# Performance work log

Hardware: AMD Instinct MI355X
Metric: run time of the kernel (lower is better)

Reference implementation:

```python
import jax, jax.numpy as jnp
import numpy as np


def setup_inputs() -> dict:
    key = jax.random.key(0)
    k1, k2, k3 = jax.random.split(key, 3)
    B, F0, D = 8192, 39, 16
    L = 128
    hash_x = jax.random.normal(k1, (B, F0, D), dtype=jnp.float32)
    W0 = jax.random.normal(k2, (F0 * F0, L), dtype=jnp.float32) * 0.05
    W1 = jax.random.normal(k3, (F0 * (L // 2), L), dtype=jnp.float32) * 0.05
    return {"hash_x": hash_x, "W0": W0, "W1": W1}


def reference(hash_x, W0, W1):
    # CIN (Compressed Interaction Network) with layer sizes [128, 128], no bias.
    x0 = hash_x                      # [B, F0, D]
    B, F0, D = x0.shape
    L = W0.shape[1]                  # 128

    # --- layer 0 ---
    # outer product over fields per embedding dim: [B, D, F0, F0] -> flatten (i,j) row-major
    z0 = jnp.einsum('bid,bjd->bdij', x0, x0).reshape(B, D, F0 * F0)
    # conv1d with kernel width 1 == matmul over flattened field-pair dim
    cur0 = jax.nn.relu(jnp.einsum('bdk,kl->bld', z0, W0))   # [B, L, D]
    next_h, direct0 = jnp.split(cur0, 2, axis=1)            # each [B, L/2, D]

    # --- layer 1 (final) ---
    Fk = next_h.shape[1]                                     # L/2 = 64
    z1 = jnp.einsum('bid,bjd->bdij', x0, next_h).reshape(B, D, F0 * Fk)
    cur1 = jax.nn.relu(jnp.einsum('bdk,kl->bld', z1, W1))   # [B, L, D]

    result = jnp.concatenate([direct0, cur1], axis=1)        # [B, L/2 + L, D]
    return jnp.sum(result, axis=-1)                          # [B, 192]
```

## Files before the change

### kernel.cpp

```cpp
#include <hip/hip_runtime.h>
#include <hip/hip_bf16.h>


using short8 = __attribute__((ext_vector_type(8))) short;
using f32x16 = __attribute__((ext_vector_type(16))) float;

#define VS 56
#define V_BYTES (256 * VS * 2)
#define HS 72
#define H_BYTES (256 * HS * 2)
#define BB_OFF (V_BYTES + H_BYTES)
#define SMEM_BYTES (BB_OFF + 8192)

#define NSL0 120
#define NSL1 156
#define NSL  (NSL0 + NSL1)
#define NFRAG (NSL * 256)

__device__ __forceinline__ unsigned short f2bf(float x) {
  __hip_bfloat16 h = __float2bfloat16(x);
  return __builtin_bit_cast(unsigned short, h);
}
__device__ __forceinline__ unsigned cvt2(float lo, float hi) {
  unsigned r;
  asm("v_cvt_pk_bf16_f32 %0, %1, %2" : "=v"(r) : "v"(lo), "v"(hi));
  return r;
}
__device__ __forceinline__ float bf_lo(unsigned w) {
  return __builtin_bit_cast(float, w << 16);
}
__device__ __forceinline__ float bf_hi(unsigned w) {
  return __builtin_bit_cast(float, w & 0xffff0000u);
}
__device__ __forceinline__ float bf2f(unsigned short b) {
  return __builtin_bit_cast(float, ((unsigned)b) << 16);
}
__device__ __forceinline__ short8 mk_a(float vi, uint4 p) {
  uint4 pk;
  pk.x = cvt2(vi * bf_lo(p.x), vi * bf_hi(p.x));
  pk.y = cvt2(vi * bf_lo(p.y), vi * bf_hi(p.y));
  pk.z = cvt2(vi * bf_lo(p.z), vi * bf_hi(p.z));
  pk.w = cvt2(vi * bf_lo(p.w), vi * bf_hi(p.w));
  return __builtin_bit_cast(short8, pk);
}
__device__ __forceinline__ void stage16(const void* g, char* l) {
  __builtin_amdgcn_global_load_lds((const __attribute__((address_space(1))) void*)g,
                                   (__attribute__((address_space(3))) void*)l, 16, 0, 0);
}

__global__ void pack_w(const float* __restrict__ W0, const float* __restrict__ W1,
                       short8* __restrict__ wpk) {
  int fid = blockIdx.x * 256 + threadIdx.x;
  if (fid >= NFRAG) return;
  int lane = fid & 63;
  int t2 = fid >> 6;
  int nb = t2 & 3, s = t2 >> 2;
  int n = nb * 32 + (lane & 31);
  int kb = (lane >> 5) * 8;
  short8 frag;
  #pragma unroll
  for (int ii = 0; ii < 8; ii++) {
    float val;
    if (s < NSL0) {
      int k = s * 16 + kb + ii;
      int i = k / 48, j = k - i * 48;
      val = (i < 39 && j < 39) ? W0[(i * 39 + j) * 128 + n] : 0.f;
    } else {
      int k = (s - NSL0) * 16 + kb + ii;
      int i = k >> 6, j = k & 63;
      val = W1[(i * 64 + j) * 128 + n];
    }
    frag[ii] = (short)f2bf(val);
  }
  wpk[fid] = frag;
}

__global__ __launch_bounds__(256, 2) void cin_main(const float* __restrict__ X,
                                                   const short8* __restrict__ wpk,
                                                   float* __restrict__ out) {
  extern __shared__ char smem[];
  unsigned short* Vb = (unsigned short*)smem;
  unsigned short* H  = (unsigned short*)(smem + V_BYTES);
  char* Bsm          = smem + BB_OFF;

  const int t    = threadIdx.x;
  const int lane = t & 63;
  const int w    = t >> 6;
  const int l31  = lane & 31, hi = lane >> 5;
  const int b0   = blockIdx.x * 16;

  const float* xb = X + (size_t)b0 * 624;
  for (int f = t * 4; f < 9984; f += 1024) {
    float4 v4 = *(const float4*)(xb + f);
    int bl = f / 624;
    int rem = f - bl * 624;
    int i = rem >> 4, d0 = rem & 15;
    int r = bl * 16 + d0;
    Vb[(r + 0) * VS + i] = f2bf(v4.x);
    Vb[(r + 1) * VS + i] = f2bf(v4.y);
    Vb[(r + 2) * VS + i] = f2bf(v4.z);
    Vb[(r + 3) * VS + i] = f2bf(v4.w);
  }
  #pragma unroll
  for (int c = 39; c < VS; c++) Vb[t * VS + c] = 0;

  stage16((const char*)wpk + ((size_t)0 * 256 + w * 64 + lane) * 16, Bsm + (w << 10));
  asm volatile("s_waitcnt vmcnt(0)" ::: "memory");
  __syncthreads();

  const int row0 = w * 64 + l31;
  const int row1 = row0 + 32;

  uint4 vp0[3], vp1[3];
  #pragma unroll
  for (int rr = 0; rr < 3; rr++) {
    vp0[rr] = *(const uint4*)(Vb + row0 * VS + 16 * rr + 8 * hi);
    vp1[rr] = *(const uint4*)(Vb + row1 * VS + 16 * rr + 8 * hi);
  }

  f32x16 acc[2][4];
  #pragma unroll
  for (int mi = 0; mi < 2; mi++)
    #pragma unroll
    for (int nb = 0; nb < 4; nb++)
      #pragma unroll
      for (int e = 0; e < 16; e++) acc[mi][nb][e] = 0.f;

  int sg = 0;
  #pragma unroll 1
  for (int ig = 0; ig < 40; ig++) {
    float vi0 = bf2f(Vb[row0 * VS + ig]);
    float vi1 = bf2f(Vb[row1 * VS + ig]);
    #pragma unroll
    for (int rr = 0; rr < 3; rr++) {
      stage16((const char*)wpk + ((size_t)(sg + 1) * 256 + w * 64 + lane) * 16,
              Bsm + (((sg + 1) & 1) << 12) + (w << 10));
      const char* bb = Bsm + ((sg & 1) << 12) + (lane << 4);
      short8 bf0 = *(const short8*)(bb + 0);
      short8 bf1 = *(const short8*)(bb + 1024);
      short8 bf2 = *(const short8*)(bb + 2048);
      short8 bf3 = *(const short8*)(bb + 3072);
      short8 a0 = mk_a(vi0, vp0[rr]);
      short8 a1 = mk_a(vi1, vp1[rr]);
      acc[0][0] = __builtin_amdgcn_mfma_f32_32x32x16_bf16(a0, bf0, acc[0][0], 0, 0, 0);
      acc[1][0] = __builtin_amdgcn_mfma_f32_32x32x16_bf16(a1, bf0, acc[1][0], 0, 0, 0);
      acc[0][1] = __builtin_amdgcn_mfma_f32_32x32x16_bf16(a0, bf1, acc[0][1], 0, 0, 0);
      acc[1][1] = __builtin_amdgcn_mfma_f32_32x32x16_bf16(a1, bf1, acc[1][1], 0, 0, 0);
      acc[0][2] = __builtin_amdgcn_mfma_f32_32x32x16_bf16(a0, bf2, acc[0][2], 0, 0, 0);
      acc[1][2] = __builtin_amdgcn_mfma_f32_32x32x16_bf16(a1, bf2, acc[1][2], 0, 0, 0);
      acc[0][3] = __builtin_amdgcn_mfma_f32_32x32x16_bf16(a0, bf3, acc[0][3], 0, 0, 0);
      acc[1][3] = __builtin_amdgcn_mfma_f32_32x32x16_bf16(a1, bf3, acc[1][3], 0, 0, 0);
      asm volatile("s_waitcnt vmcnt(0)" ::: "memory");
      __syncthreads();
      sg++;
    }
  }

  #pragma unroll
  for (int mi = 0; mi < 2; mi++)
    #pragma unroll
    for (int nb = 0; nb < 2; nb++)
      #pragma unroll
      for (int r = 0; r < 16; r++) {
        int rt = (r & 3) + 8 * (r >> 2) + 4 * hi;
        H[(w * 64 + mi * 32 + rt) * HS + nb * 32 + l31] = f2bf(fmaxf(acc[mi][nb][r], 0.f));
      }
  #pragma unroll
  for (int mi = 0; mi < 2; mi++)
    #pragma unroll
    for (int nb = 2; nb < 4; nb++) {
      float s0 = 0.f, s1 = 0.f;
      #pragma unroll
      for (int r = 0; r < 8; r++)  s0 += fmaxf(acc[mi][nb][r], 0.f);
      #pragma unroll
      for (int r = 8; r < 16; r++) s1 += fmaxf(acc[mi][nb][r], 0.f);
      s0 += __shfl_xor(s0, 32);
      s1 += __shfl_xor(s1, 32);
      out[(size_t)(b0 + 4 * w + 2 * mi + hi) * 192 + (nb - 2) * 32 + l31] = hi ? s1 : s0;
    }
  __syncthreads();

  uint4 hp0[4], hp1[4];
  #pragma unroll
  for (int rr = 0; rr < 4; rr++) {
    hp0[rr] = *(const uint4*)(H + row0 * HS + 16 * rr + 8 * hi);
    hp1[rr] = *(const uint4*)(H + row1 * HS + 16 * rr + 8 * hi);
  }

  #pragma unroll
  for (int mi = 0; mi < 2; mi++)
    #pragma unroll
    for (int nb = 0; nb < 4; nb++)
      #pragma unroll
      for (int e = 0; e < 16; e++) acc[mi][nb][e] = 0.f;

  #pragma unroll 1
  for (int ig = 0; ig < 39; ig++) {
    float vi0 = bf2f(Vb[row0 * VS + ig]);
    float vi1 = bf2f(Vb[row1 * VS + ig]);
    #pragma unroll
    for (int rr = 0; rr < 4; rr++) {
      if (sg + 1 < NSL)
        stage16((const char*)wpk + ((size_t)(sg + 1) * 256 + w * 64 + lane) * 16,
                Bsm + (((sg + 1) & 1) << 12) + (w << 10));
      const char* bb = Bsm + ((sg & 1) << 12) + (lane << 4);
      short8 bf0 = *(const short8*)(bb + 0);
      short8 bf1 = *(const short8*)(bb + 1024);
      short8 bf2 = *(const short8*)(bb + 2048);
      short8 bf3 = *(const short8*)(bb + 3072);
      short8 a0 = mk_a(vi0, hp0[rr]);
      short8 a1 = mk_a(vi1, hp1[rr]);
      acc[0][0] = __builtin_amdgcn_mfma_f32_32x32x16_bf16(a0, bf0, acc[0][0], 0, 0, 0);
      acc[1][0] = __builtin_amdgcn_mfma_f32_32x32x16_bf16(a1, bf0, acc[1][0], 0, 0, 0);
      acc[0][1] = __builtin_amdgcn_mfma_f32_32x32x16_bf16(a0, bf1, acc[0][1], 0, 0, 0);
      acc[1][1] = __builtin_amdgcn_mfma_f32_32x32x16_bf16(a1, bf1, acc[1][1], 0, 0, 0);
      acc[0][2] = __builtin_amdgcn_mfma_f32_32x32x16_bf16(a0, bf2, acc[0][2], 0, 0, 0);
      acc[1][2] = __builtin_amdgcn_mfma_f32_32x32x16_bf16(a1, bf2, acc[1][2], 0, 0, 0);
      acc[0][3] = __builtin_amdgcn_mfma_f32_32x32x16_bf16(a0, bf3, acc[0][3], 0, 0, 0);
      acc[1][3] = __builtin_amdgcn_mfma_f32_32x32x16_bf16(a1, bf3, acc[1][3], 0, 0, 0);
      asm volatile("s_waitcnt vmcnt(0)" ::: "memory");
      __syncthreads();
      sg++;
    }
  }

  #pragma unroll
  for (int mi = 0; mi < 2; mi++)
    #pragma unroll
    for (int nb = 0; nb < 4; nb++) {
      float s0 = 0.f, s1 = 0.f;
      #pragma unroll
      for (int r = 0; r < 8; r++)  s0 += fmaxf(acc[mi][nb][r], 0.f);
      #pragma unroll
      for (int r = 8; r < 16; r++) s1 += fmaxf(acc[mi][nb][r], 0.f);
      s0 += __shfl_xor(s0, 32);
      s1 += __shfl_xor(s1, 32);
      out[(size_t)(b0 + 4 * w + 2 * mi + hi) * 192 + 64 + nb * 32 + l31] = hi ? s1 : s0;
    }
}

extern "C" void kernel_launch(void* const* d_in, const int* in_sizes, int n_in,
                              void* d_out, int out_size, void* d_ws, size_t ws_size,
                              hipStream_t stream) {
  (void)in_sizes; (void)n_in; (void)out_size; (void)ws_size;
  const float* X  = (const float*)d_in[0];
  const float* W0 = (const float*)d_in[1];
  const float* W1 = (const float*)d_in[2];
  float* out = (float*)d_out;
  short8* wpk = (short8*)d_ws;

  (void)hipFuncSetAttribute((const void*)cin_main,
                            hipFuncAttributeMaxDynamicSharedMemorySize, SMEM_BYTES);

  pack_w<<<(NFRAG + 255) / 256, 256, 0, stream>>>(W0, W1, wpk);
  cin_main<<<512, 256, SMEM_BYTES, stream>>>(X, wpk, out);
}
```

Measured before the change: 188.4 us.

## Triple-buffer weight staging and repack layer-0 K with tighter padding

Layer 0's K dimension is repacked with a field stride of 40 instead of 48, so it needs 100 K-slices instead of 120. Each iteration now covers two i-fields across five 16-wide chunks, which removes padded MFMA work. Weight staging moves from double to triple buffering with a prefetch distance of two, and the loop waits only on the older load (vmcnt(1)) before a bare s_barrier. Initial staging is issued before the X load so it overlaps. The risks are the extra LDS buffer, more selection logic when building A fragments, and the weaker waitcnt/barrier combination, which is correct only if the LDS visibility assumptions hold.

```diff
diff --git a/kernel.cpp b/kernel.cpp
--- a/kernel.cpp
+++ b/kernel.cpp
@@ -10,9 +10,9 @@
 #define HS 72
 #define H_BYTES (256 * HS * 2)
 #define BB_OFF (V_BYTES + H_BYTES)
-#define SMEM_BYTES (BB_OFF + 8192)
-
-#define NSL0 120
+#define SMEM_BYTES (BB_OFF + 3 * 4096)
+
+#define NSL0 100
 #define NSL1 156
 #define NSL  (NSL0 + NSL1)
 #define NFRAG (NSL * 256)
@@ -63,7 +63,7 @@
     float val;
     if (s < NSL0) {
       int k = s * 16 + kb + ii;
-      int i = k / 48, j = k - i * 48;
+      int i = k / 40, j = k - i * 40;
       val = (i < 39 && j < 39) ? W0[(i * 39 + j) * 128 + n] : 0.f;
     } else {
       int k = (s - NSL0) * 16 + kb + ii;
@@ -88,6 +88,11 @@
   const int w    = t >> 6;
   const int l31  = lane & 31, hi = lane >> 5;
   const int b0   = blockIdx.x * 16;
+  const char* wpkc = (const char*)wpk;
+  const int stoff = (w * 64 + lane) * 16;
+
+  stage16(wpkc + 0 * 4096 + stoff, Bsm + 0 * 4096 + (w << 10));
+  stage16(wpkc + 1 * 4096 + stoff, Bsm + 1 * 4096 + (w << 10));
 
   const float* xb = X + (size_t)b0 * 624;
   for (int f = t * 4; f < 9984; f += 1024) {
@@ -103,19 +108,18 @@
   }
   #pragma unroll
   for (int c = 39; c < VS; c++) Vb[t * VS + c] = 0;
-
-  stage16((const char*)wpk + ((size_t)0 * 256 + w * 64 + lane) * 16, Bsm + (w << 10));
-  asm volatile("s_waitcnt vmcnt(0)" ::: "memory");
   __syncthreads();
 
   const int row0 = w * 64 + l31;
   const int row1 = row0 + 32;
-
-  uint4 vp0[3], vp1[3];
-  #pragma unroll
-  for (int rr = 0; rr < 3; rr++) {
-    vp0[rr] = *(const uint4*)(Vb + row0 * VS + 16 * rr + 8 * hi);
-    vp1[rr] = *(const uint4*)(Vb + row1 * VS + 16 * rr + 8 * hi);
+  const int hi8  = 8 * hi;
+
+  uint4 vpe0[5], vpe1[5];
+  #pragma unroll
+  for (int rr = 0; rr < 5; rr++) {
+    int j0 = (16 * rr + hi8) % 40;
+    vpe0[rr] = *(const uint4*)(Vb + row0 * VS + j0);
+    vpe1[rr] = *(const uint4*)(Vb + row1 * VS + j0);
   }
 
   f32x16 acc[2][4];
@@ -126,22 +130,26 @@
       #pragma unroll
       for (int e = 0; e < 16; e++) acc[mi][nb][e] = 0.f;
 
-  int sg = 0;
+  int sg = 0, bcur = 0;
   #pragma unroll 1
-  for (int ig = 0; ig < 40; ig++) {
-    float vi0 = bf2f(Vb[row0 * VS + ig]);
-    float vi1 = bf2f(Vb[row1 * VS + ig]);
-    #pragma unroll
-    for (int rr = 0; rr < 3; rr++) {
-      stage16((const char*)wpk + ((size_t)(sg + 1) * 256 + w * 64 + lane) * 16,
-              Bsm + (((sg + 1) & 1) << 12) + (w << 10));
-      const char* bb = Bsm + ((sg & 1) << 12) + (lane << 4);
+  for (int m = 0; m < 20; m++) {
+    float viA0 = bf2f(Vb[row0 * VS + 2 * m]);
+    float viB0 = bf2f(Vb[row0 * VS + 2 * m + 1]);
+    float viA1 = bf2f(Vb[row1 * VS + 2 * m]);
+    float viB1 = bf2f(Vb[row1 * VS + 2 * m + 1]);
+    #pragma unroll
+    for (int rr = 0; rr < 5; rr++) {
+      int bst = bcur + 2; if (bst >= 3) bst -= 3;
+      stage16(wpkc + (size_t)(sg + 2) * 4096 + stoff, Bsm + (bst << 12) + (w << 10));
+      const char* bb = Bsm + (bcur << 12) + (lane << 4);
       short8 bf0 = *(const short8*)(bb + 0);
       short8 bf1 = *(const short8*)(bb + 1024);
       short8 bf2 = *(const short8*)(bb + 2048);
       short8 bf3 = *(const short8*)(bb + 3072);
-      short8 a0 = mk_a(vi0, vp0[rr]);
-      short8 a1 = mk_a(vi1, vp1[rr]);
+      float vi0 = (rr < 2) ? viA0 : (rr > 2) ? viB0 : (hi ? viB0 : viA0);
+      float vi1 = (rr < 2) ? viA1 : (rr > 2) ? viB1 : (hi ? viB1 : viA1);
+      short8 a0 = mk_a(vi0, vpe0[rr]);
+      short8 a1 = mk_a(vi1, vpe1[rr]);
       acc[0][0] = __builtin_amdgcn_mfma_f32_32x32x16_bf16(a0, bf0, acc[0][0], 0, 0, 0);
       acc[1][0] = __builtin_amdgcn_mfma_f32_32x32x16_bf16(a1, bf0, acc[1][0], 0, 0, 0);
       acc[0][1] = __builtin_amdgcn_mfma_f32_32x32x16_bf16(a0, bf1, acc[0][1], 0, 0, 0);
@@ -150,9 +158,11 @@
       acc[1][2] = __builtin_amdgcn_mfma_f32_32x32x16_bf16(a1, bf2, acc[1][2], 0, 0, 0);
       acc[0][3] = __builtin_amdgcn_mfma_f32_32x32x16_bf16(a0, bf3, acc[0][3], 0, 0, 0);
       acc[1][3] = __builtin_amdgcn_mfma_f32_32x32x16_bf16(a1, bf3, acc[1][3], 0, 0, 0);
-      asm volatile("s_waitcnt vmcnt(0)" ::: "memory");
-      __syncthreads();
-      sg++;
+      asm volatile("s_waitcnt vmcnt(1)" ::: "memory");
+      __builtin_amdgcn_sched_barrier(0);
+      __builtin_amdgcn_s_barrier();
+      __builtin_amdgcn_sched_barrier(0);
+      sg++; bcur = bcur + 1 == 3 ? 0 : bcur + 1;
     }
   }
 
@@ -183,8 +193,8 @@
   uint4 hp0[4], hp1[4];
   #pragma unroll
   for (int rr = 0; rr < 4; rr++) {
-    hp0[rr] = *(const uint4*)(H + row0 * HS + 16 * rr + 8 * hi);
-    hp1[rr] = *(const uint4*)(H + row1 * HS + 16 * rr + 8 * hi);
+    hp0[rr] = *(const uint4*)(H + row0 * HS + 16 * rr + hi8);
+    hp1[rr] = *(const uint4*)(H + row1 * HS + 16 * rr + hi8);
   }
 
   #pragma unroll
@@ -200,10 +210,10 @@
     float vi1 = bf2f(Vb[row1 * VS + ig]);
     #pragma unroll
     for (int rr = 0; rr < 4; rr++) {
-      if (sg + 1 < NSL)
-        stage16((const char*)wpk + ((size_t)(sg + 1) * 256 + w * 64 + lane) * 16,
-                Bsm + (((sg + 1) & 1) << 12) + (w << 10));
-      const char* bb = Bsm + ((sg & 1) << 12) + (lane << 4);
+      int bst = bcur + 2; if (bst >= 3) bst -= 3;
+      if (sg + 2 < NSL)
+        stage16(wpkc + (size_t)(sg + 2) * 4096 + stoff, Bsm + (bst << 12) + (w << 10));
+      const char* bb = Bsm + (bcur << 12) + (lane << 4);
       short8 bf0 = *(const short8*)(bb + 0);
       short8 bf1 = *(const short8*)(bb + 1024);
       short8 bf2 = *(const short8*)(bb + 2048);
@@ -218,9 +228,11 @@
       acc[1][2] = __builtin_amdgcn_mfma_f32_32x32x16_bf16(a1, bf2, acc[1][2], 0, 0, 0);
       acc[0][3] = __builtin_amdgcn_mfma_f32_32x32x16_bf16(a0, bf3, acc[0][3], 0, 0, 0);
       acc[1][3] = __builtin_amdgcn_mfma_f32_32x32x16_bf16(a1, bf3, acc[1][3], 0, 0, 0);
-      asm volatile("s_waitcnt vmcnt(0)" ::: "memory");
-      __syncthreads();
-      sg++;
+      asm volatile("s_waitcnt vmcnt(1)" ::: "memory");
+      __builtin_amdgcn_sched_barrier(0);
+      __builtin_amdgcn_s_barrier();
+      __builtin_amdgcn_sched_barrier(0);
+      sg++; bcur = bcur + 1 == 3 ? 0 : bcur + 1;
     }
   }
 
```

Measured after the change: 189.9 us. About the same (+0.8%).
